# Optimization experiments

Measured on AMD Instinct MI355X. Metric: run time of the kernel, lower is better.

The kernel has to match this reference:

```python
import jax, jax.numpy as jnp
import numpy as np

EMBED_DIM = 512
NUM_HEADS = 8
HEAD_DIM = EMBED_DIM // NUM_HEADS
SCALING = HEAD_DIM ** (-0.5)
LAMBDA = 1.0
T = 128
B = 8


def setup_inputs() -> dict:
    key = jax.random.key(0)
    ks = jax.random.split(key, 8)
    d = EMBED_DIM
    # xavier-uniform-ish scale for weights
    w_lim = float(np.sqrt(6.0 / (3 * d + d)))
    o_lim = float(np.sqrt(6.0 / (d + d)))
    return {
        "query": jax.random.normal(ks[0], (T, B, d), jnp.float32),
        "key": jax.random.normal(ks[1], (T, B, d), jnp.float32),
        "value": jax.random.normal(ks[2], (T, B, d), jnp.float32),
        "correlation_bias": jax.random.normal(ks[3], (B, T, T, T), jnp.float32) * 0.1,
        "in_proj_weight": jax.random.uniform(ks[4], (3 * d, d), jnp.float32, -w_lim, w_lim),
        "in_proj_bias": jnp.zeros((3 * d,), jnp.float32),
        "out_w": jax.random.uniform(ks[5], (d, d), jnp.float32, -o_lim, o_lim),
        "out_b": jnp.zeros((d,), jnp.float32),
    }


def reference(query, key, value, correlation_bias, in_proj_weight, in_proj_bias, out_w, out_b):
    tgt_len, bsz, d = query.shape
    h, hd = NUM_HEADS, HEAD_DIM
    # split packed in-projection
    q = query @ in_proj_weight[:d].T + in_proj_bias[:d]
    k = key @ in_proj_weight[d:2 * d].T + in_proj_bias[d:2 * d]
    v = value @ in_proj_weight[2 * d:].T + in_proj_bias[2 * d:]
    q = q * SCALING
    # [T, B, D] -> [B*H, T, hd]
    q = q.reshape(tgt_len, bsz * h, hd).transpose(1, 0, 2)
    k = k.reshape(tgt_len, bsz * h, hd).transpose(1, 0, 2)
    v = v.reshape(tgt_len, bsz * h, hd).transpose(1, 0, 2)
    # trilinear score cube: [B*H, Tq, Tk, Tv]
    scores = jnp.einsum('iat,ibt,ict->iabc', q, k, v)
    # expand correlation bias over heads: [B,Tq,Tk,Tv] -> [B*H,Tq,Tk,Tv]
    bias = jnp.broadcast_to(
        correlation_bias[:, None], (bsz, h, tgt_len, tgt_len, tgt_len)
    ).reshape(bsz * h, tgt_len, tgt_len, tgt_len)
    scores = scores + LAMBDA * bias
    # mean/max fusion over Tv, softmax over Tk
    fused = jnp.mean(scores, axis=-1) + jnp.max(scores, axis=-1)
    w = jax.nn.softmax(fused.astype(jnp.float32), axis=-1).astype(fused.dtype)
    # bmm with q (note: attends over q itself, Tk == Tq required)
    attn = jnp.einsum('iab,ibd->iad', w, q)
    attn = attn.transpose(1, 0, 2).reshape(tgt_len, bsz, d)
    return attn @ out_w.T + out_b
```

## Files before the change

### kernel.cpp

```cpp
#include <hip/hip_runtime.h>
#include <math.h>

#define SCALING 0.125f

typedef __attribute__((ext_vector_type(8))) short short8;
typedef __attribute__((ext_vector_type(4))) float f32x4;

static __device__ __forceinline__ unsigned short bf16r(float x) {
  unsigned int u = __float_as_uint(x);
  u += 0x7fffu + ((u >> 16) & 1u);
  return (unsigned short)(u >> 16);
}
static __device__ __forceinline__ unsigned int pk_bf16(float lo, float hi) {
  unsigned int ua = __float_as_uint(lo);
  unsigned int ub = __float_as_uint(hi);
  ua += 0x7fffu + ((ua >> 16) & 1u);
  ub += 0x7fffu + ((ub >> 16) & 1u);
  return __builtin_amdgcn_perm(ub, ua, 0x07060302u);
}

__global__ __launch_bounds__(256)
void proj_kernel(const float* __restrict__ query,
                 const float* __restrict__ key,
                 const float* __restrict__ value,
                 const float* __restrict__ W,
                 const float* __restrict__ bias,
                 float* __restrict__ qh,
                 float* __restrict__ kh,
                 unsigned short* __restrict__ vh) {
  __shared__ float Xs[16][68];
  __shared__ float Ws[16][68];
  const int r0 = blockIdx.y * 64;
  const int c0 = blockIdx.x * 64;
  const int g = c0 >> 9;
  const float* __restrict__ X = (g == 0) ? query : (g == 1) ? key : value;
  const int tid = threadIdx.x;
  const int lrow = tid >> 2;
  const int lk4 = (tid & 3) * 4;
  const int tr = tid >> 4;
  const int tc = tid & 15;

  float acc[4][4] = {};
  float4 xv = *(const float4*)&X[(r0 + lrow) * 512 + lk4];
  float4 wv = *(const float4*)&W[(c0 + lrow) * 512 + lk4];
  for (int kt = 0; kt < 512; kt += 16) {
    __syncthreads();
    Xs[lk4 + 0][lrow] = xv.x; Xs[lk4 + 1][lrow] = xv.y;
    Xs[lk4 + 2][lrow] = xv.z; Xs[lk4 + 3][lrow] = xv.w;
    Ws[lk4 + 0][lrow] = wv.x; Ws[lk4 + 1][lrow] = wv.y;
    Ws[lk4 + 2][lrow] = wv.z; Ws[lk4 + 3][lrow] = wv.w;
    __syncthreads();
    if (kt + 16 < 512) {
      xv = *(const float4*)&X[(r0 + lrow) * 512 + kt + 16 + lk4];
      wv = *(const float4*)&W[(c0 + lrow) * 512 + kt + 16 + lk4];
    }
#pragma unroll
    for (int kk = 0; kk < 16; kk++) {
      float a[4], b[4];
      *(float4*)a = *(const float4*)&Xs[kk][tr * 4];
      *(float4*)b = *(const float4*)&Ws[kk][tc * 4];
#pragma unroll
      for (int ri = 0; ri < 4; ri++)
#pragma unroll
        for (int cj = 0; cj < 4; cj++)
          acc[ri][cj] = fmaf(a[ri], b[cj], acc[ri][cj]);
    }
  }

#pragma unroll
  for (int ri = 0; ri < 4; ri++) {
    const int r = r0 + tr * 4 + ri;
    const int t = r >> 3;
    const int batch = r & 7;
#pragma unroll
    for (int cj = 0; cj < 4; cj++) {
      const int j = c0 + tc * 4 + cj;
      float val = acc[ri][cj] + bias[j];
      const int jj = j & 511;
      const int head = jj >> 6;
      const int hd = jj & 63;
      const int i = batch * 8 + head;
      const int idx = ((i << 7) + t) * 64 + hd;
      if (g == 0)      qh[idx] = val * SCALING;
      else if (g == 1) kh[idx] = val;
      else             vh[idx] = bf16r(val);
    }
  }
}

__global__ __launch_bounds__(256)
void score_kernel(const float* __restrict__ qh,
                  const float* __restrict__ kh,
                  const unsigned short* __restrict__ vh,
                  const float* __restrict__ cbias,
                  float* __restrict__ fused) {
  __shared__ __align__(16) unsigned short Ks[64 * 72];
  __shared__ __align__(16) unsigned short Vs[128 * 72];

  const int bid = blockIdx.x;
  const int bh = bid & 1;
  const int ab = bid >> 1;
  const int batch = ab >> 7;
  const int a = ab & 127;
  const int tid = threadIdx.x;
  const int w = tid >> 6;
  const int lane = tid & 63;
  const int quad = lane >> 4;
  const int n15 = lane & 15;
  const int col8 = (tid & 7) * 8;
  const int bglob = bh * 64 + w * 16 + n15;

  const float* __restrict__ bp = cbias + (size_t)ab * 16384;

  for (int h = 0; h < 8; ++h) {
    const int i = batch * 8 + h;
    const float* __restrict__ kb = kh + (size_t)i * 8192 + (size_t)bh * 64 * 64;
    const uint4* __restrict__ vb4 = (const uint4*)(vh + (size_t)i * 8192);
    const float* __restrict__ qa = qh + ((size_t)i * 128 + a) * 64;

    f32x4 q0 = *(const f32x4*)&qa[col8];
    f32x4 q1 = *(const f32x4*)&qa[col8 + 4];
#pragma unroll
    for (int j = 0; j < 4; ++j) {
      const int gg = j * 256 + tid;
      const int row = gg >> 3;
      *(uint4*)&Vs[row * 72 + col8] = vb4[gg];
    }
#pragma unroll
    for (int j = 0; j < 2; ++j) {
      const int gg = j * 256 + tid;
      const int row = gg >> 3;
      f32x4 k0 = *(const f32x4*)&kb[8 * gg];
      f32x4 k1 = *(const f32x4*)&kb[8 * gg + 4];
      k0 *= q0;
      k1 *= q1;
      uint4 pk;
      pk.x = pk_bf16(k0[0], k0[1]);
      pk.y = pk_bf16(k0[2], k0[3]);
      pk.z = pk_bf16(k1[0], k1[1]);
      pk.w = pk_bf16(k1[2], k1[3]);
      *(uint4*)&Ks[row * 72 + col8] = pk;
    }
    __syncthreads();

    short8 bf0 = *(const short8*)&Ks[(w * 16 + n15) * 72 + quad * 8];
    short8 bf1 = *(const short8*)&Ks[(w * 16 + n15) * 72 + 32 + quad * 8];

    f32x4 acc[8];
#pragma unroll
    for (int ic = 0; ic < 8; ++ic) acc[ic] = (f32x4){0.f, 0.f, 0.f, 0.f};
#pragma unroll
    for (int ic = 0; ic < 8; ++ic) {
      short8 a0 = *(const short8*)&Vs[(ic * 16 + n15) * 72 + quad * 8];
      short8 a1 = *(const short8*)&Vs[(ic * 16 + n15) * 72 + 32 + quad * 8];
      acc[ic] = __builtin_amdgcn_mfma_f32_16x16x32_bf16(a0, bf0, acc[ic], 0, 0, 0);
      acc[ic] = __builtin_amdgcn_mfma_f32_16x16x32_bf16(a1, bf1, acc[ic], 0, 0, 0);
    }
    __syncthreads();

    float fsum = 0.f, fmx = -INFINITY;
#pragma unroll
    for (int ic = 0; ic < 8; ++ic) {
      f32x4 bb = *(const f32x4*)&bp[bglob * 128 + ic * 16 + quad * 4];
#pragma unroll
      for (int r = 0; r < 4; ++r) {
        const float v = acc[ic][r] + bb[r];
        fsum += v;
        fmx = fmaxf(fmx, v);
      }
    }
    fsum += __shfl_xor(fsum, 16, 64);
    fmx = fmaxf(fmx, __shfl_xor(fmx, 16, 64));
    fsum += __shfl_xor(fsum, 32, 64);
    fmx = fmaxf(fmx, __shfl_xor(fmx, 32, 64));
    if (quad == 0)
      fused[((size_t)i * 128 + a) * 128 + bglob] = fsum * (1.0f / 128.0f) + fmx;
  }
}

__global__ __launch_bounds__(64)
void softmax_attn_kernel(const float* __restrict__ fused,
                         const float* __restrict__ qh,
                         float* __restrict__ attn) {
  const int bid = blockIdx.x;
  const int i = bid >> 7;
  const int a = bid & 127;
  const int lane = threadIdx.x;
  const float* __restrict__ fr = fused + (size_t)bid * 128;
  float f0 = fr[lane], f1 = fr[lane + 64];
  float m = fmaxf(f0, f1);
#pragma unroll
  for (int off = 32; off >= 1; off >>= 1) m = fmaxf(m, __shfl_xor(m, off, 64));
  const float e0 = expf(f0 - m), e1 = expf(f1 - m);
  float s = e0 + e1;
#pragma unroll
  for (int off = 32; off >= 1; off >>= 1) s += __shfl_xor(s, off, 64);
  const float inv = 1.0f / s;
  __shared__ float w[128];
  w[lane] = e0 * inv;
  w[lane + 64] = e1 * inv;
  __syncthreads();
  const float* __restrict__ qp = qh + (size_t)i * 128 * 64 + lane;
  float acc = 0.0f;
#pragma unroll 4
  for (int b = 0; b < 128; b++) acc = fmaf(w[b], qp[b * 64], acc);
  const int batch = i >> 3, head = i & 7;
  attn[((size_t)a * 8 + batch) * 512 + head * 64 + lane] = acc;
}

__global__ __launch_bounds__(256)
void outproj_kernel(const float* __restrict__ Xa,
                    const float* __restrict__ W,
                    const float* __restrict__ bias,
                    float* __restrict__ out) {
  __shared__ float Xs[16][68];
  __shared__ float Ws[16][68];
  const int r0 = blockIdx.y * 64;
  const int c0 = blockIdx.x * 64;
  const int tid = threadIdx.x;
  const int lrow = tid >> 2;
  const int lk4 = (tid & 3) * 4;
  const int tr = tid >> 4;
  const int tc = tid & 15;

  float acc[4][4] = {};
  float4 xv = *(const float4*)&Xa[(r0 + lrow) * 512 + lk4];
  float4 wv = *(const float4*)&W[(c0 + lrow) * 512 + lk4];
  for (int kt = 0; kt < 512; kt += 16) {
    __syncthreads();
    Xs[lk4 + 0][lrow] = xv.x; Xs[lk4 + 1][lrow] = xv.y;
    Xs[lk4 + 2][lrow] = xv.z; Xs[lk4 + 3][lrow] = xv.w;
    Ws[lk4 + 0][lrow] = wv.x; Ws[lk4 + 1][lrow] = wv.y;
    Ws[lk4 + 2][lrow] = wv.z; Ws[lk4 + 3][lrow] = wv.w;
    __syncthreads();
    if (kt + 16 < 512) {
      xv = *(const float4*)&Xa[(r0 + lrow) * 512 + kt + 16 + lk4];
      wv = *(const float4*)&W[(c0 + lrow) * 512 + kt + 16 + lk4];
    }
#pragma unroll
    for (int kk = 0; kk < 16; kk++) {
      float a[4], b[4];
      *(float4*)a = *(const float4*)&Xs[kk][tr * 4];
      *(float4*)b = *(const float4*)&Ws[kk][tc * 4];
#pragma unroll
      for (int ri = 0; ri < 4; ri++)
#pragma unroll
        for (int cj = 0; cj < 4; cj++)
          acc[ri][cj] = fmaf(a[ri], b[cj], acc[ri][cj]);
    }
  }
#pragma unroll
  for (int ri = 0; ri < 4; ri++) {
    const int r = r0 + tr * 4 + ri;
#pragma unroll
    for (int cj = 0; cj < 4; cj++) {
      const int j = c0 + tc * 4 + cj;
      out[(size_t)r * 512 + j] = acc[ri][cj] + bias[j];
    }
  }
}

extern "C" void kernel_launch(void* const* d_in, const int* in_sizes, int n_in,
                              void* d_out, int out_size, void* d_ws,
                              size_t ws_size, hipStream_t stream) {
  const float* query = (const float*)d_in[0];
  const float* key   = (const float*)d_in[1];
  const float* value = (const float*)d_in[2];
  const float* cbias = (const float*)d_in[3];
  const float* W     = (const float*)d_in[4];
  const float* pb    = (const float*)d_in[5];
  const float* out_w = (const float*)d_in[6];
  const float* out_b = (const float*)d_in[7];
  float* out = (float*)d_out;

  float* ws = (float*)d_ws;
  float* qh = ws;
  float* kh = ws + 524288;
  unsigned short* vh = (unsigned short*)(ws + 1048576);
  float* fusedb = ws + 1048576 + 262144;
  float* attn = fusedb + 1048576;

  proj_kernel<<<dim3(24, 16), 256, 0, stream>>>(query, key, value, W, pb, qh,
                                                kh, vh);
  score_kernel<<<2048, 256, 0, stream>>>(qh, kh, vh, cbias, fusedb);
  softmax_attn_kernel<<<8192, 64, 0, stream>>>(fusedb, qh, attn);
  outproj_kernel<<<dim3(8, 16), 256, 0, stream>>>(attn, out_w, out_b, out);
}
```

Baseline: 211.8 us.

## Use split-bf16 MFMA GEMMs for projections and hoist correlation bias loads

Replaces the fp32 SIMT shared-memory GEMMs for the input and output projections with MFMA GEMMs. These use a hi/lo bf16 split (three MFMAs per tile) to approximate fp32 accuracy. A new conversion kernel pre-splits the inputs and weights, and the softmax kernel now writes attn as hi/lo bf16. The score kernel loads its correlation-bias slice into registers once, instead of re-reading it for each of the 8 heads. The cost is an extra launch, extra memory traffic for the converted copies, and workspace aliasing between the fused buffer and the converted arrays.

```diff
diff --git a/kernel.cpp b/kernel.cpp
--- a/kernel.cpp
+++ b/kernel.cpp
@@ -10,6 +10,9 @@
   unsigned int u = __float_as_uint(x);
   u += 0x7fffu + ((u >> 16) & 1u);
   return (unsigned short)(u >> 16);
+}
+static __device__ __forceinline__ float bf16f(unsigned short h) {
+  return __uint_as_float(((unsigned int)h) << 16);
 }
 static __device__ __forceinline__ unsigned int pk_bf16(float lo, float hi) {
   unsigned int ua = __float_as_uint(lo);
@@ -20,67 +23,82 @@
 }
 
 __global__ __launch_bounds__(256)
-void proj_kernel(const float* __restrict__ query,
-                 const float* __restrict__ key,
-                 const float* __restrict__ value,
-                 const float* __restrict__ W,
-                 const float* __restrict__ bias,
-                 float* __restrict__ qh,
-                 float* __restrict__ kh,
-                 unsigned short* __restrict__ vh) {
-  __shared__ float Xs[16][68];
-  __shared__ float Ws[16][68];
-  const int r0 = blockIdx.y * 64;
-  const int c0 = blockIdx.x * 64;
-  const int g = c0 >> 9;
-  const float* __restrict__ X = (g == 0) ? query : (g == 1) ? key : value;
-  const int tid = threadIdx.x;
-  const int lrow = tid >> 2;
-  const int lk4 = (tid & 3) * 4;
-  const int tr = tid >> 4;
-  const int tc = tid & 15;
-
-  float acc[4][4] = {};
-  float4 xv = *(const float4*)&X[(r0 + lrow) * 512 + lk4];
-  float4 wv = *(const float4*)&W[(c0 + lrow) * 512 + lk4];
-  for (int kt = 0; kt < 512; kt += 16) {
-    __syncthreads();
-    Xs[lk4 + 0][lrow] = xv.x; Xs[lk4 + 1][lrow] = xv.y;
-    Xs[lk4 + 2][lrow] = xv.z; Xs[lk4 + 3][lrow] = xv.w;
-    Ws[lk4 + 0][lrow] = wv.x; Ws[lk4 + 1][lrow] = wv.y;
-    Ws[lk4 + 2][lrow] = wv.z; Ws[lk4 + 3][lrow] = wv.w;
-    __syncthreads();
-    if (kt + 16 < 512) {
-      xv = *(const float4*)&X[(r0 + lrow) * 512 + kt + 16 + lk4];
-      wv = *(const float4*)&W[(c0 + lrow) * 512 + kt + 16 + lk4];
-    }
-#pragma unroll
-    for (int kk = 0; kk < 16; kk++) {
-      float a[4], b[4];
-      *(float4*)a = *(const float4*)&Xs[kk][tr * 4];
-      *(float4*)b = *(const float4*)&Ws[kk][tc * 4];
-#pragma unroll
-      for (int ri = 0; ri < 4; ri++)
-#pragma unroll
-        for (int cj = 0; cj < 4; cj++)
-          acc[ri][cj] = fmaf(a[ri], b[cj], acc[ri][cj]);
-    }
-  }
-
-#pragma unroll
-  for (int ri = 0; ri < 4; ri++) {
-    const int r = r0 + tr * 4 + ri;
-    const int t = r >> 3;
-    const int batch = r & 7;
-#pragma unroll
-    for (int cj = 0; cj < 4; cj++) {
-      const int j = c0 + tc * 4 + cj;
-      float val = acc[ri][cj] + bias[j];
-      const int jj = j & 511;
-      const int head = jj >> 6;
-      const int hd = jj & 63;
+void convert_kernel(const float* __restrict__ q, const float* __restrict__ k,
+                    const float* __restrict__ v, const float* __restrict__ W,
+                    const float* __restrict__ ow,
+                    unsigned short* __restrict__ hi,
+                    unsigned short* __restrict__ lo) {
+  const int base = blockIdx.x * 1024 + threadIdx.x * 4;
+  const float* src;
+  int off = base;
+  if (base < 524288)       { src = q; }
+  else if (base < 1048576) { src = k;  off = base - 524288; }
+  else if (base < 1572864) { src = v;  off = base - 1048576; }
+  else if (base < 2359296) { src = W;  off = base - 1572864; }
+  else                     { src = ow; off = base - 2359296; }
+  float4 x = *(const float4*)&src[off];
+  ushort4 h, l;
+  h.x = bf16r(x.x); l.x = bf16r(x.x - bf16f(h.x));
+  h.y = bf16r(x.y); l.y = bf16r(x.y - bf16f(h.y));
+  h.z = bf16r(x.z); l.z = bf16r(x.z - bf16f(h.z));
+  h.w = bf16r(x.w); l.w = bf16r(x.w - bf16f(h.w));
+  *(ushort4*)&hi[base] = h;
+  *(ushort4*)&lo[base] = l;
+}
+
+__global__ __launch_bounds__(256)
+void projmm_kernel(const unsigned short* __restrict__ cvt_hi,
+                   const unsigned short* __restrict__ cvt_lo,
+                   const float* __restrict__ bias,
+                   float* __restrict__ qh, float* __restrict__ kh,
+                   unsigned short* __restrict__ vh) {
+  const int n0 = blockIdx.x * 64;
+  const int g = n0 >> 9;
+  const int w = threadIdx.x >> 6;
+  const int lane = threadIdx.x & 63;
+  const int quad = lane >> 4, n15 = lane & 15;
+  const int m0 = blockIdx.y * 64 + w * 16;
+
+  const unsigned short* __restrict__ Ah = cvt_hi + g * 524288;
+  const unsigned short* __restrict__ Al = cvt_lo + g * 524288;
+  const unsigned short* __restrict__ Bh = cvt_hi + 1572864;
+  const unsigned short* __restrict__ Bl = cvt_lo + 1572864;
+
+  f32x4 acc[4];
+#pragma unroll
+  for (int nt = 0; nt < 4; ++nt) acc[nt] = (f32x4){0.f, 0.f, 0.f, 0.f};
+
+  const int arow = (m0 + n15) * 512;
+  for (int k0 = 0; k0 < 512; k0 += 32) {
+    const int kq = k0 + quad * 8;
+    short8 ah = *(const short8*)&Ah[arow + kq];
+    short8 al = *(const short8*)&Al[arow + kq];
+#pragma unroll
+    for (int nt = 0; nt < 4; ++nt) {
+      const int brow = (n0 + nt * 16 + n15) * 512;
+      short8 bh = *(const short8*)&Bh[brow + kq];
+      short8 bl = *(const short8*)&Bl[brow + kq];
+      acc[nt] = __builtin_amdgcn_mfma_f32_16x16x32_bf16(ah, bh, acc[nt], 0, 0, 0);
+      acc[nt] = __builtin_amdgcn_mfma_f32_16x16x32_bf16(ah, bl, acc[nt], 0, 0, 0);
+      acc[nt] = __builtin_amdgcn_mfma_f32_16x16x32_bf16(al, bh, acc[nt], 0, 0, 0);
+    }
+  }
+
+#pragma unroll
+  for (int nt = 0; nt < 4; ++nt) {
+    const int j = n0 + nt * 16 + n15;
+    const int jj = j & 511;
+    const int head = jj >> 6;
+    const int hd = jj & 63;
+    const float bj = bias[j];
+#pragma unroll
+    for (int r = 0; r < 4; ++r) {
+      const int row = m0 + quad * 4 + r;
+      const int t = row >> 3;
+      const int batch = row & 7;
       const int i = batch * 8 + head;
       const int idx = ((i << 7) + t) * 64 + hd;
+      const float val = acc[nt][r] + bj;
       if (g == 0)      qh[idx] = val * SCALING;
       else if (g == 1) kh[idx] = val;
       else             vh[idx] = bf16r(val);
@@ -111,6 +129,10 @@
   const int bglob = bh * 64 + w * 16 + n15;
 
   const float* __restrict__ bp = cbias + (size_t)ab * 16384;
+  f32x4 biasReg[8];
+#pragma unroll
+  for (int ic = 0; ic < 8; ++ic)
+    biasReg[ic] = *(const f32x4*)&bp[bglob * 128 + ic * 16 + quad * 4];
 
   for (int h = 0; h < 8; ++h) {
     const int i = batch * 8 + h;
@@ -161,10 +183,9 @@
     float fsum = 0.f, fmx = -INFINITY;
 #pragma unroll
     for (int ic = 0; ic < 8; ++ic) {
-      f32x4 bb = *(const f32x4*)&bp[bglob * 128 + ic * 16 + quad * 4];
 #pragma unroll
       for (int r = 0; r < 4; ++r) {
-        const float v = acc[ic][r] + bb[r];
+        const float v = acc[ic][r] + biasReg[ic][r];
         fsum += v;
         fmx = fmaxf(fmx, v);
       }
@@ -181,7 +202,8 @@
 __global__ __launch_bounds__(64)
 void softmax_attn_kernel(const float* __restrict__ fused,
                          const float* __restrict__ qh,
-                         float* __restrict__ attn) {
+                         unsigned short* __restrict__ attn_hi,
+                         unsigned short* __restrict__ attn_lo) {
   const int bid = blockIdx.x;
   const int i = bid >> 7;
   const int a = bid & 127;
@@ -205,57 +227,56 @@
 #pragma unroll 4
   for (int b = 0; b < 128; b++) acc = fmaf(w[b], qp[b * 64], acc);
   const int batch = i >> 3, head = i & 7;
-  attn[((size_t)a * 8 + batch) * 512 + head * 64 + lane] = acc;
+  const int idx = ((int)(a * 8 + batch)) * 512 + head * 64 + lane;
+  const unsigned short h = bf16r(acc);
+  attn_hi[idx] = h;
+  attn_lo[idx] = bf16r(acc - bf16f(h));
 }
 
 __global__ __launch_bounds__(256)
-void outproj_kernel(const float* __restrict__ Xa,
-                    const float* __restrict__ W,
-                    const float* __restrict__ bias,
-                    float* __restrict__ out) {
-  __shared__ float Xs[16][68];
-  __shared__ float Ws[16][68];
-  const int r0 = blockIdx.y * 64;
-  const int c0 = blockIdx.x * 64;
-  const int tid = threadIdx.x;
-  const int lrow = tid >> 2;
-  const int lk4 = (tid & 3) * 4;
-  const int tr = tid >> 4;
-  const int tc = tid & 15;
-
-  float acc[4][4] = {};
-  float4 xv = *(const float4*)&Xa[(r0 + lrow) * 512 + lk4];
-  float4 wv = *(const float4*)&W[(c0 + lrow) * 512 + lk4];
-  for (int kt = 0; kt < 512; kt += 16) {
-    __syncthreads();
-    Xs[lk4 + 0][lrow] = xv.x; Xs[lk4 + 1][lrow] = xv.y;
-    Xs[lk4 + 2][lrow] = xv.z; Xs[lk4 + 3][lrow] = xv.w;
-    Ws[lk4 + 0][lrow] = wv.x; Ws[lk4 + 1][lrow] = wv.y;
-    Ws[lk4 + 2][lrow] = wv.z; Ws[lk4 + 3][lrow] = wv.w;
-    __syncthreads();
-    if (kt + 16 < 512) {
-      xv = *(const float4*)&Xa[(r0 + lrow) * 512 + kt + 16 + lk4];
-      wv = *(const float4*)&W[(c0 + lrow) * 512 + kt + 16 + lk4];
-    }
-#pragma unroll
-    for (int kk = 0; kk < 16; kk++) {
-      float a[4], b[4];
-      *(float4*)a = *(const float4*)&Xs[kk][tr * 4];
-      *(float4*)b = *(const float4*)&Ws[kk][tc * 4];
-#pragma unroll
-      for (int ri = 0; ri < 4; ri++)
-#pragma unroll
-        for (int cj = 0; cj < 4; cj++)
-          acc[ri][cj] = fmaf(a[ri], b[cj], acc[ri][cj]);
-    }
-  }
-#pragma unroll
-  for (int ri = 0; ri < 4; ri++) {
-    const int r = r0 + tr * 4 + ri;
-#pragma unroll
-    for (int cj = 0; cj < 4; cj++) {
-      const int j = c0 + tc * 4 + cj;
-      out[(size_t)r * 512 + j] = acc[ri][cj] + bias[j];
+void outmm_kernel(const unsigned short* __restrict__ attn_hi,
+                  const unsigned short* __restrict__ attn_lo,
+                  const unsigned short* __restrict__ cvt_hi,
+                  const unsigned short* __restrict__ cvt_lo,
+                  const float* __restrict__ bias,
+                  float* __restrict__ out) {
+  const int n0 = blockIdx.x * 64;
+  const int w = threadIdx.x >> 6;
+  const int lane = threadIdx.x & 63;
+  const int quad = lane >> 4, n15 = lane & 15;
+  const int m0 = blockIdx.y * 64 + w * 16;
+
+  const unsigned short* __restrict__ Bh = cvt_hi + 2359296;
+  const unsigned short* __restrict__ Bl = cvt_lo + 2359296;
+
+  f32x4 acc[4];
+#pragma unroll
+  for (int nt = 0; nt < 4; ++nt) acc[nt] = (f32x4){0.f, 0.f, 0.f, 0.f};
+
+  const int arow = (m0 + n15) * 512;
+  for (int k0 = 0; k0 < 512; k0 += 32) {
+    const int kq = k0 + quad * 8;
+    short8 ah = *(const short8*)&attn_hi[arow + kq];
+    short8 al = *(const short8*)&attn_lo[arow + kq];
+#pragma unroll
+    for (int nt = 0; nt < 4; ++nt) {
+      const int brow = (n0 + nt * 16 + n15) * 512;
+      short8 bh = *(const short8*)&Bh[brow + kq];
+      short8 bl = *(const short8*)&Bl[brow + kq];
+      acc[nt] = __builtin_amdgcn_mfma_f32_16x16x32_bf16(ah, bh, acc[nt], 0, 0, 0);
+      acc[nt] = __builtin_amdgcn_mfma_f32_16x16x32_bf16(ah, bl, acc[nt], 0, 0, 0);
+      acc[nt] = __builtin_amdgcn_mfma_f32_16x16x32_bf16(al, bh, acc[nt], 0, 0, 0);
+    }
+  }
+
+#pragma unroll
+  for (int nt = 0; nt < 4; ++nt) {
+    const int j = n0 + nt * 16 + n15;
+    const float bj = bias[j];
+#pragma unroll
+    for (int r = 0; r < 4; ++r) {
+      const int row = m0 + quad * 4 + r;
+      out[(size_t)row * 512 + j] = acc[nt][r] + bj;
     }
   }
 }
@@ -277,12 +298,18 @@
   float* qh = ws;
   float* kh = ws + 524288;
   unsigned short* vh = (unsigned short*)(ws + 1048576);
-  float* fusedb = ws + 1048576 + 262144;
-  float* attn = fusedb + 1048576;
-
-  proj_kernel<<<dim3(24, 16), 256, 0, stream>>>(query, key, value, W, pb, qh,
-                                                kh, vh);
+  unsigned short* cvt_hi = (unsigned short*)(ws + 1310720);
+  unsigned short* cvt_lo = (unsigned short*)(ws + 2621440);
+  float* fusedb = (float*)cvt_hi;
+  unsigned short* attn_hi = cvt_lo;
+  unsigned short* attn_lo = cvt_lo + 524288;
+
+  convert_kernel<<<2560, 256, 0, stream>>>(query, key, value, W, out_w,
+                                           cvt_hi, cvt_lo);
+  projmm_kernel<<<dim3(24, 16), 256, 0, stream>>>(cvt_hi, cvt_lo, pb, qh, kh,
+                                                  vh);
   score_kernel<<<2048, 256, 0, stream>>>(qh, kh, vh, cbias, fusedb);
-  softmax_attn_kernel<<<8192, 64, 0, stream>>>(fusedb, qh, attn);
-  outproj_kernel<<<dim3(8, 16), 256, 0, stream>>>(attn, out_w, out_b, out);
-}
+  softmax_attn_kernel<<<8192, 64, 0, stream>>>(fusedb, qh, attn_hi, attn_lo);
+  outmm_kernel<<<dim3(8, 16), 256, 0, stream>>>(attn_hi, attn_lo, cvt_hi,
+                                                cvt_lo, out_b, out);
+}
```

Result: slower. 220.6 us (+4.2%).
